# Kernel optimization log

Hardware: AMD Instinct MI355X
Metric: run time of the kernel (lower is better)

The kernel has to match this reference:

```python
import jax, jax.numpy as jnp
import numpy as np

EPS = 1e-5
K = 20


def _knn_idx(p, k):
    # p: (B, N, C) -> indices of k nearest neighbors (B, N, k), self included
    inner = jnp.einsum('bnc,bmc->bnm', p, p)
    sq = jnp.sum(p * p, axis=-1)  # (B, N)
    neg_dist = 2.0 * inner - sq[:, :, None] - sq[:, None, :]
    return jax.lax.top_k(neg_dist, k)[1]


def _edge_feature(x, k):
    # x: (B, N, C) -> (B, N, k, 2C) = [neighbor - center, center]
    C = x.shape[-1]
    src = x if C in (3, 6) else x[..., 6:9]  # faithful to torch code path
    idx = _knn_idx(src, k)                    # (B, N, k)
    nb = jax.vmap(lambda xb, ib: xb[ib])(x, idx)  # (B, N, k, C)
    ctr = jnp.broadcast_to(x[:, :, None, :], nb.shape)
    return jnp.concatenate([nb - ctr, ctr], axis=-1)


def _block(h, W, g, b, m, v):
    # 1x1 conv (channels-last) + eval-mode BatchNorm + LeakyReLU(0.2)
    z = jnp.einsum('...c,oc->...o', h, W)
    z = (z - m) * jax.lax.rsqrt(v + EPS) * g + b
    return jnp.where(z >= 0, z, 0.2 * z)


def setup_inputs() -> dict:
    key = jax.random.key(0)
    B, N, D, F = 8, 2048, 3, 1024
    ks = jax.random.split(key, 16)
    s = 0.1
    x = jax.random.normal(ks[0], (B, N, D), dtype=jnp.float32)
    W1 = jax.random.normal(ks[1], (64, 2 * D), dtype=jnp.float32) * s
    W2 = jax.random.normal(ks[2], (64, 64), dtype=jnp.float32) * s
    W3 = jax.random.normal(ks[3], (64, 128), dtype=jnp.float32) * s
    W4 = jax.random.normal(ks[4], (64, 64), dtype=jnp.float32) * s
    W5 = jax.random.normal(ks[5], (64, 128), dtype=jnp.float32) * s
    W6 = jax.random.normal(ks[6], (F, 192), dtype=jnp.float32) * s
    # BN params for bn1..bn5 stacked along axis 0
    bng = 1.0 + 0.1 * jax.random.normal(ks[7], (5, 64), dtype=jnp.float32)
    bnb = 0.1 * jax.random.normal(ks[8], (5, 64), dtype=jnp.float32)
    bnm = 0.1 * jax.random.normal(ks[9], (5, 64), dtype=jnp.float32)
    bnv = 0.5 + jax.random.uniform(ks[10], (5, 64), dtype=jnp.float32)
    bn6g = 1.0 + 0.1 * jax.random.normal(ks[11], (F,), dtype=jnp.float32)
    bn6b = 0.1 * jax.random.normal(ks[12], (F,), dtype=jnp.float32)
    bn6m = 0.1 * jax.random.normal(ks[13], (F,), dtype=jnp.float32)
    bn6v = 0.5 + jax.random.uniform(ks[14], (F,), dtype=jnp.float32)
    return {"x": x, "W1": W1, "W2": W2, "W3": W3, "W4": W4, "W5": W5,
            "W6": W6, "bng": bng, "bnb": bnb, "bnm": bnm, "bnv": bnv,
            "bn6g": bn6g, "bn6b": bn6b, "bn6m": bn6m, "bn6v": bn6v}


def reference(x, W1, W2, W3, W4, W5, W6, bng, bnb, bnm, bnv,
              bn6g, bn6b, bn6m, bn6v):
    # x: (B, N, 3) channels-last throughout
    e = _edge_feature(x, K)                    # (B, N, K, 6)
    h = _block(e, W1, bng[0], bnb[0], bnm[0], bnv[0])
    h = _block(h, W2, bng[1], bnb[1], bnm[1], bnv[1])
    x1 = jnp.max(h, axis=2)                    # (B, N, 64)

    e = _edge_feature(x1, K)                   # knn on channels 6:9
    h = _block(e, W3, bng[2], bnb[2], bnm[2], bnv[2])
    h = _block(h, W4, bng[3], bnb[3], bnm[3], bnv[3])
    x2 = jnp.max(h, axis=2)                    # (B, N, 64)

    e = _edge_feature(x2, K)
    h = _block(e, W5, bng[4], bnb[4], bnm[4], bnv[4])
    x3 = jnp.max(h, axis=2)                    # (B, N, 64)

    x4 = jnp.concatenate([x1, x2, x3], axis=-1)  # (B, N, 192)
    z = _block(x4, W6, bn6g, bn6b, bn6m, bn6v)   # (B, N, F)
    g = jnp.max(z, axis=1)                       # (B, F)
    feat = g[:, None, :]                         # (B, 1, F)
    return feat, jnp.transpose(x4, (0, 2, 1))    # x4 as (B, 192, N)
```

## Files before the change

### kernel.cpp

```cpp
#include <hip/hip_runtime.h>
#include <hip/hip_bf16.h>
#include <math.h>

#define B_ 8
#define N_ 2048
#define KNN 20
#define CH 64

typedef unsigned int u32;
typedef unsigned short ushort16;
typedef __attribute__((ext_vector_type(8))) short s8v;
typedef __attribute__((ext_vector_type(4))) float f4v;

__device__ __forceinline__ float lrelu(float z) { return z >= 0.0f ? z : 0.2f * z; }

__device__ __forceinline__ u32 enc_f32(float f) {
  u32 u = __float_as_uint(f);
  return (u & 0x80000000u) ? ~u : (u | 0x80000000u);
}
__device__ __forceinline__ float dec_f32(u32 u) {
  u32 bits = (u & 0x80000000u) ? (u ^ 0x80000000u) : ~u;
  return __uint_as_float(bits);
}
__device__ __forceinline__ ushort16 f2bf(float f) {
  u32 u = __float_as_uint(f);
  u = (u + 0x7fffu + ((u >> 16) & 1u)) >> 16;
  return (ushort16)u;
}
__device__ __forceinline__ float bf2f(ushort16 h) { return __uint_as_float(((u32)h) << 16); }

__device__ __forceinline__ void split3(const float* __restrict__ p, s8v& a0, s8v& a1, s8v& a2) {
#pragma unroll
  for (int j = 0; j < 8; ++j) {
    float v = p[j];
    ushort16 h0 = f2bf(v);
    float r = v - bf2f(h0);
    u32 ru = __float_as_uint(r);
    a0[j] = (short)h0;
    a1[j] = (short)(ru >> 16);
    float r2 = r - __uint_as_float(ru & 0xFFFF0000u);
    a2[j] = (short)f2bf(r2);
  }
}

#define MFMA6(ACC, A0, A1, A2, B0, B1, B2)                                   \
  ACC = __builtin_amdgcn_mfma_f32_16x16x32_bf16(A0, B0, ACC, 0, 0, 0);       \
  ACC = __builtin_amdgcn_mfma_f32_16x16x32_bf16(A0, B1, ACC, 0, 0, 0);       \
  ACC = __builtin_amdgcn_mfma_f32_16x16x32_bf16(A1, B0, ACC, 0, 0, 0);       \
  ACC = __builtin_amdgcn_mfma_f32_16x16x32_bf16(A0, B2, ACC, 0, 0, 0);       \
  ACC = __builtin_amdgcn_mfma_f32_16x16x32_bf16(A1, B1, ACC, 0, 0, 0);       \
  ACC = __builtin_amdgcn_mfma_f32_16x16x32_bf16(A2, B0, ACC, 0, 0, 0);

__device__ __forceinline__ void wsplit(float v, ushort16& h0, ushort16& h1, ushort16& h2) {
  h0 = f2bf(v);
  float r = v - bf2f(h0);
  h1 = f2bf(r);
  float r2 = r - bf2f(h1);
  h2 = f2bf(r2);
}

__global__ __launch_bounds__(256) void prep_kernel(
    const float* __restrict__ W2, const float* __restrict__ W3, const float* __restrict__ W4,
    const float* __restrict__ W5, const float* __restrict__ W6,
    float* __restrict__ w2tg, float* __restrict__ w3tg, float* __restrict__ w4tg,
    ushort16* __restrict__ wp5h, ushort16* __restrict__ wp5m, ushort16* __restrict__ wp5l,
    float* __restrict__ w6t, u32* __restrict__ gkeys) {
  int i = blockIdx.x * 256 + threadIdx.x;
  if (i < 192 * 1024) {
    int d = i >> 10, cc = i & 1023;
    w6t[i] = W6[cc * 192 + d];
  }
  if (i < 4096) {
    int c_ = i >> 6, cc = i & 63;
    w2tg[cc * 64 + c_] = W2[i];
    w4tg[cc * 64 + c_] = W4[i];
  }
  if (i < 8192) {
    gkeys[i] = 0u;
    { int d = i >> 6, c_ = i & 63; w3tg[i] = W3[c_ * 128 + d]; }
    int j = i & 7, l = (i >> 3) & 63, tile = i >> 9;
    int kk = tile >> 2, nt = tile & 3;
    int d = kk * 32 + ((l >> 4) << 3) + j;
    int ch = nt * 16 + (l & 15);
    float v5 = (d < 64) ? W5[ch * 128 + d] : (W5[ch * 128 + d] - W5[ch * 128 + d - 64]);
    ushort16 a, b, c;
    wsplit(v5, a, b, c); wp5h[i] = a; wp5m[i] = b; wp5l[i] = c;
  }
}

#define QPB 32
#define SL 8
#define CSL (N_ / SL)
#define CAP 31

__global__ __launch_bounds__(256) void knn_kernel(const float* __restrict__ p, int ld, int off,
                                                  int* __restrict__ idxout) {
  __shared__ __align__(16) char arena[64640];
  float4* pts = (float4*)arena;
  int* buf = (int*)(arena + 32896);
  double* dls = (double*)arena;
  int* ils = (int*)(arena + 40960);

  const int b = blockIdx.y;
  const float* pb = p + (size_t)b * N_ * ld + off;
  for (int j = threadIdx.x; j < N_; j += 256) {
    pts[j + (j >> 8)] = make_float4(pb[(size_t)j * ld + 0], pb[(size_t)j * ld + 1],
                                    pb[(size_t)j * ld + 2], 0.f);
  }
  __syncthreads();

  const int t = threadIdx.x & 7;
  const int qloc = threadIdx.x >> 3;
  const int q = blockIdx.x * QPB + qloc;
  const float4 qp = pts[q + (q >> 8)];
  const int jb = t * CSL;
  const float4* myp = pts + jb + t;

  float d0 = 1e30f, d1 = 1e30f, d2 = 1e30f;
#pragma unroll 4
  for (int i = 0; i < CSL; ++i) {
    float4 c = myp[i];
    float dx = qp.x - c.x, dy = qp.y - c.y, dz = qp.z - c.z;
    float d = fmaf(dz, dz, fmaf(dy, dy, dx * dx));
    float lo = fminf(d, d0); float hi = fmaxf(d, d0); d0 = lo;
    float m1 = fminf(d1, hi); float c1 = fmaxf(d1, hi); d1 = m1;
    d2 = fminf(d2, c1);
  }
  float thr = d2;
#pragma unroll
  for (int s = 1; s < 8; s <<= 1) thr = fmaxf(thr, __shfl_xor(thr, s));
  thr = thr * 1.0001f + 1e-7f;

  int cnt = 0;
  int* mybuf = buf + threadIdx.x * CAP;
#pragma unroll 4
  for (int i = 0; i < CSL; ++i) {
    float4 c = myp[i];
    float dx = qp.x - c.x, dy = qp.y - c.y, dz = qp.z - c.z;
    float d = fmaf(dz, dz, fmaf(dy, dy, dx * dx));
    if (d <= thr) {
      if (cnt < CAP) mybuf[cnt] = jb + i;
      ++cnt;
    }
  }

  double ld_[KNN]; int li_[KNN];
#pragma unroll
  for (int u = 0; u < KNN; ++u) { ld_[u] = 1e300; li_[u] = 0x7fffffff; }

  const bool ovf = cnt > CAP;
  const int m = ovf ? 0 : cnt;
  for (int e = 0; e < m; ++e) {
    int j = mybuf[e];
    float4 c = pts[j + (j >> 8)];
    double dx = (double)qp.x - (double)c.x;
    double dy = (double)qp.y - (double)c.y;
    double dz = (double)qp.z - (double)c.z;
    double d = dx * dx + dy * dy + dz * dz;
    if (d < ld_[KNN - 1]) {
      ld_[KNN - 1] = d; li_[KNN - 1] = j;
#pragma unroll
      for (int u = KNN - 1; u > 0; --u) {
        if (ld_[u] < ld_[u - 1]) {
          double td = ld_[u]; ld_[u] = ld_[u - 1]; ld_[u - 1] = td;
          int ti = li_[u]; li_[u] = li_[u - 1]; li_[u - 1] = ti;
        }
      }
    }
  }
  if (ovf) {
    for (int i = 0; i < CSL; ++i) {
      int j = jb + i;
      float4 c = myp[i];
      double dx = (double)qp.x - (double)c.x;
      double dy = (double)qp.y - (double)c.y;
      double dz = (double)qp.z - (double)c.z;
      double d = dx * dx + dy * dy + dz * dz;
      if (d < ld_[KNN - 1]) {
        ld_[KNN - 1] = d; li_[KNN - 1] = j;
#pragma unroll
        for (int u = KNN - 1; u > 0; --u) {
          if (ld_[u] < ld_[u - 1]) {
            double td = ld_[u]; ld_[u] = ld_[u - 1]; ld_[u - 1] = td;
            int ti = li_[u]; li_[u] = li_[u - 1]; li_[u - 1] = ti;
          }
        }
      }
    }
  }
  __syncthreads();
#pragma unroll
  for (int u = 0; u < KNN; ++u) {
    dls[threadIdx.x * KNN + u] = ld_[u];
    ils[threadIdx.x * KNN + u] = li_[u];
  }
  __syncthreads();

  if (t == 0) {
    int h0 = 0, h1 = 0, h2 = 0, h3 = 0, h4 = 0, h5 = 0, h6 = 0, h7 = 0;
    const int lb = qloc * 8;
    int* outp = idxout + ((size_t)b * N_ + q) * KNN;
    for (int r = 0; r < KNN; ++r) {
      double bd = 1e301; int bi = 0x7fffffff; int bt = 0;
#define CONSIDER(T, H)                                                     \
      { int li2 = (lb + (T)) * KNN + (H);                                  \
        double dv = dls[li2]; int iv = ils[li2];                           \
        if (dv < bd || (dv == bd && iv < bi)) { bd = dv; bi = iv; bt = (T); } }
      CONSIDER(0, h0) CONSIDER(1, h1) CONSIDER(2, h2) CONSIDER(3, h3)
      CONSIDER(4, h4) CONSIDER(5, h5) CONSIDER(6, h6) CONSIDER(7, h7)
#undef CONSIDER
      outp[r] = bi;
      h0 += (bt == 0); h1 += (bt == 1); h2 += (bt == 2); h3 += (bt == 3);
      h4 += (bt == 4); h5 += (bt == 5); h6 += (bt == 6); h7 += (bt == 7);
    }
  }
}

__global__ __launch_bounds__(256) void stage1_kernel(
    const float* __restrict__ x, const int* __restrict__ idx,
    const float* __restrict__ W1, const float* __restrict__ w2tg,
    const float* __restrict__ g0, const float* __restrict__ b0,
    const float* __restrict__ m0, const float* __restrict__ v0,
    const float* __restrict__ g1, const float* __restrict__ b1,
    const float* __restrict__ m1, const float* __restrict__ v1,
    float* __restrict__ x1out) {
  __shared__ float nbs[4][KNN][3];
  __shared__ float ctrs[4][3];
  __shared__ int sidx[4][KNN];
  const int b = blockIdx.y;
  const int n0 = blockIdx.x * 4;
  const int p = threadIdx.x >> 6, c = threadIdx.x & 63;

  for (int i = threadIdx.x; i < 4 * KNN; i += 256)
    sidx[i / KNN][i % KNN] = idx[((size_t)b * N_ + n0 + i / KNN) * KNN + i % KNN];
  __syncthreads();
  for (int i = threadIdx.x; i < 4 * KNN * 3; i += 256) {
    int pp = i / (KNN * 3), r = i % (KNN * 3), k = r / 3, d = r % 3;
    nbs[pp][k][d] = x[((size_t)b * N_ + sidx[pp][k]) * 3 + d];
  }
  if (threadIdx.x < 12) {
    int pp = threadIdx.x / 3, d = threadIdx.x % 3;
    ctrs[pp][d] = x[((size_t)b * N_ + n0 + pp) * 3 + d];
  }
  __syncthreads();

  float sc0, sh0, sc1, sh1;
  {
    double rs = 1.0 / sqrt((double)v0[c] + 1e-5);
    sc0 = (float)((double)g0[c] * rs); sh0 = b0[c] - m0[c] * sc0;
    rs = 1.0 / sqrt((double)v1[c] + 1e-5);
    sc1 = (float)((double)g1[c] * rs); sh1 = b1[c] - m1[c] * sc1;
  }

  const float cx = ctrs[p][0], cy = ctrs[p][1], cz = ctrs[p][2];
  const float wa0 = W1[c * 6 + 0], wa1 = W1[c * 6 + 1], wa2 = W1[c * 6 + 2];
  const float wb0 = W1[c * 6 + 3], wb1 = W1[c * 6 + 4], wb2 = W1[c * 6 + 5];
  const float cbase = cx * wb0 + cy * wb1 + cz * wb2;

  float h1r[KNN];
#pragma unroll
  for (int k = 0; k < KNN; ++k) {
    float a = (nbs[p][k][0] - cx) * wa0 + (nbs[p][k][1] - cy) * wa1 + (nbs[p][k][2] - cz) * wa2 + cbase;
    h1r[k] = lrelu(a * sc0 + sh0);
  }

  float acc2[KNN];
#pragma unroll
  for (int k = 0; k < KNN; ++k) acc2[k] = 0.f;
  for (int cc = 0; cc < CH; ++cc) {
    float w = w2tg[cc * CH + c];
#pragma unroll
    for (int k = 0; k < KNN; ++k) {
      float hv = __int_as_float(__builtin_amdgcn_readlane(__float_as_int(h1r[k]), cc));
      acc2[k] += hv * w;
    }
  }
  float mx = -INFINITY;
#pragma unroll
  for (int k = 0; k < KNN; ++k) mx = fmaxf(mx, lrelu(acc2[k] * sc1 + sh1));
  x1out[((size_t)b * N_ + n0 + p) * CH + c] = mx;
}

__global__ __launch_bounds__(256) void stage2_kernel(
    const float* __restrict__ xin, const int* __restrict__ idx,
    const float* __restrict__ w3tg, const float* __restrict__ w4tg,
    const float* __restrict__ g0, const float* __restrict__ b0,
    const float* __restrict__ m0, const float* __restrict__ v0,
    const float* __restrict__ g1, const float* __restrict__ b1,
    const float* __restrict__ m1, const float* __restrict__ v1,
    float* __restrict__ xout) {
  __shared__ float nbs[4][KNN][CH];
  __shared__ float ctrs[4][CH];
  __shared__ int sidx[4][KNN];
  const int b = blockIdx.y, n0 = blockIdx.x * 4;
  const int p = threadIdx.x >> 6, c = threadIdx.x & 63;

  for (int i = threadIdx.x; i < 4 * KNN; i += 256)
    sidx[i / KNN][i % KNN] = idx[((size_t)b * N_ + n0 + i / KNN) * KNN + i % KNN];
  __syncthreads();
  for (int i = threadIdx.x; i < 4 * KNN * 16; i += 256) {
    int pp = i / (KNN * 16), r = i % (KNN * 16), k = r >> 4, d4 = (r & 15) * 4;
    const float4 v = *(const float4*)&xin[((size_t)b * N_ + sidx[pp][k]) * CH + d4];
    *(float4*)&nbs[pp][k][d4] = v;
  }
  for (int i = threadIdx.x; i < 4 * 16; i += 256) {
    int pp = i / 16, d4 = (i % 16) * 4;
    *(float4*)&ctrs[pp][d4] = *(const float4*)&xin[((size_t)b * N_ + n0 + pp) * CH + d4];
  }
  __syncthreads();

  float sc0, sh0, sc1, sh1;
  {
    double rs = 1.0 / sqrt((double)v0[c] + 1e-5);
    sc0 = (float)((double)g0[c] * rs); sh0 = b0[c] - m0[c] * sc0;
    rs = 1.0 / sqrt((double)v1[c] + 1e-5);
    sc1 = (float)((double)g1[c] * rs); sh1 = b1[c] - m1[c] * sc1;
  }

  float acc[KNN];
#pragma unroll
  for (int k = 0; k < KNN; ++k) acc[k] = 0.f;
  float base = 0.f;
#pragma unroll 4
  for (int d = 0; d < CH; d += 4) {
    float a0 = w3tg[(d + 0) * 64 + c], a1 = w3tg[(d + 1) * 64 + c];
    float a2 = w3tg[(d + 2) * 64 + c], a3 = w3tg[(d + 3) * 64 + c];
    float q0 = w3tg[(64 + d + 0) * 64 + c], q1 = w3tg[(64 + d + 1) * 64 + c];
    float q2 = w3tg[(64 + d + 2) * 64 + c], q3 = w3tg[(64 + d + 3) * 64 + c];
    const float4 ct = *(const float4*)&ctrs[p][d];
    base += ct.x * (q0 - a0) + ct.y * (q1 - a1) + ct.z * (q2 - a2) + ct.w * (q3 - a3);
#pragma unroll
    for (int k = 0; k < KNN; ++k) {
      const float4 nb = *(const float4*)&nbs[p][k][d];
      acc[k] += nb.x * a0 + nb.y * a1 + nb.z * a2 + nb.w * a3;
    }
  }
  float h1r[KNN];
#pragma unroll
  for (int k = 0; k < KNN; ++k) h1r[k] = lrelu((acc[k] + base) * sc0 + sh0);

  float acc2[KNN];
#pragma unroll
  for (int k = 0; k < KNN; ++k) acc2[k] = 0.f;
  for (int cc = 0; cc < CH; ++cc) {
    float w = w4tg[cc * CH + c];
#pragma unroll
    for (int k = 0; k < KNN; ++k) {
      float hv = __int_as_float(__builtin_amdgcn_readlane(__float_as_int(h1r[k]), cc));
      acc2[k] += hv * w;
    }
  }
  float mx = -INFINITY;
#pragma unroll
  for (int k = 0; k < KNN; ++k) mx = fmaxf(mx, lrelu(acc2[k] * sc1 + sh1));
  xout[((size_t)b * N_ + n0 + p) * CH + c] = mx;
}

__global__ __launch_bounds__(256) void stage3_kernel(
    const float* __restrict__ xf, const int* __restrict__ idx,
    const ushort16* __restrict__ wpAh, const ushort16* __restrict__ wpAm, const ushort16* __restrict__ wpAl,
    const float* __restrict__ g0, const float* __restrict__ b0,
    const float* __restrict__ m0, const float* __restrict__ v0,
    float* __restrict__ xoutf) {
  __shared__ int sidx[160];
  __shared__ u32 h2k[512];
  const int b = blockIdx.y, n0 = blockIdx.x * 8;
  const int tid = threadIdx.x, l = tid & 63, wv = tid >> 6;

  for (int i = tid; i < 160; i += 256) sidx[i] = idx[((size_t)b * N_ + n0 + i / KNN) * KNN + i % KNN];
  for (int i = tid; i < 512; i += 256) h2k[i] = 0u;
  __syncthreads();

  float sc1[4], sh1[4];
#pragma unroll
  for (int nt = 0; nt < 4; ++nt) {
    int ch = nt * 16 + (l & 15);
    double rs = 1.0 / sqrt((double)v0[ch] + 1e-5);
    sc1[nt] = (float)((double)g0[ch] * rs); sh1[nt] = b0[ch] - m0[ch] * sc1[nt];
  }
  const int lg = (l >> 4) << 3;

  for (int mt = wv; mt < 10; mt += 4) {
    const int row = mt * 16 + (l & 15);
    const int nb = sidx[row];
    const int p = row / KNN;
    const float* xnb = xf + ((size_t)b * N_ + nb) * CH;
    const float* xct = xf + ((size_t)b * N_ + n0 + p) * CH;

    f4v acc[4];
#pragma unroll
    for (int nt = 0; nt < 4; ++nt) acc[nt] = (f4v){0.f, 0.f, 0.f, 0.f};
#pragma unroll
    for (int kk = 0; kk < 4; ++kk) {
      const float* src = (kk < 2) ? (xnb + kk * 32 + lg) : (xct + (kk - 2) * 32 + lg);
      s8v a0, a1, a2;
      split3(src, a0, a1, a2);
#pragma unroll
      for (int nt = 0; nt < 4; ++nt) {
        int wo = ((kk * 4 + nt) * 64 + l) << 3;
        s8v bh = *(const s8v*)&wpAh[wo];
        s8v bm = *(const s8v*)&wpAm[wo];
        s8v bl = *(const s8v*)&wpAl[wo];
        MFMA6(acc[nt], a0, a1, a2, bh, bm, bl)
      }
    }
#pragma unroll
    for (int nt = 0; nt < 4; ++nt)
#pragma unroll
      for (int r = 0; r < 4; ++r) {
        float v = lrelu(acc[nt][r] * sc1[nt] + sh1[nt]);
        int row2 = mt * 16 + ((l >> 4) << 2) + r;
        atomicMax(&h2k[(row2 / KNN) * 64 + nt * 16 + (l & 15)], enc_f32(v));
      }
  }
  __syncthreads();
  for (int i = tid; i < 512; i += 256) {
    size_t o = ((size_t)b * N_ + n0 + (i >> 6)) * CH + (i & 63);
    xoutf[o] = dec_f32(h2k[i]);
  }
}

__global__ __launch_bounds__(256) void stage6_kernel(
    const float* __restrict__ x1, const float* __restrict__ x2, const float* __restrict__ x3,
    const float* __restrict__ w6t,
    const float* __restrict__ g6, const float* __restrict__ b6,
    const float* __restrict__ m6, const float* __restrict__ v6,
    u32* __restrict__ gkeys) {
  __shared__ float xsT[192][16];
  const int b = blockIdx.y;
  const int n0 = blockIdx.x * 16;
  for (int i = threadIdx.x; i < 16 * 192; i += 256) {
    int d = i >> 4, pp = i & 15;
    float v;
    if (d < 64)       v = x1[((size_t)b * N_ + n0 + pp) * CH + d];
    else if (d < 128) v = x2[((size_t)b * N_ + n0 + pp) * CH + (d - 64)];
    else              v = x3[((size_t)b * N_ + n0 + pp) * CH + (d - 128)];
    xsT[d][pp] = v;
  }
  __syncthreads();

  const int c0 = threadIdx.x << 2;
  float4 acc[16];
#pragma unroll
  for (int pp = 0; pp < 16; ++pp) acc[pp] = make_float4(0.f, 0.f, 0.f, 0.f);

  for (int d = 0; d < 192; ++d) {
    const float4 w = *(const float4*)&w6t[(size_t)d * 1024 + c0];
#pragma unroll
    for (int q = 0; q < 4; ++q) {
      const float4 xq = *(const float4*)&xsT[d][q * 4];
#define ACC4(J, XV) { float4& A = acc[q * 4 + (J)]; A.x += (XV) * w.x; A.y += (XV) * w.y; A.z += (XV) * w.z; A.w += (XV) * w.w; }
      ACC4(0, xq.x) ACC4(1, xq.y) ACC4(2, xq.z) ACC4(3, xq.w)
#undef ACC4
    }
  }

  const float4 gg = *(const float4*)&g6[c0];
  const float4 bb = *(const float4*)&b6[c0];
  const float4 mm = *(const float4*)&m6[c0];
  const float4 vv = *(const float4*)&v6[c0];
  float4 s, h;
  s.x = (float)((double)gg.x / sqrt((double)vv.x + 1e-5)); h.x = bb.x - mm.x * s.x;
  s.y = (float)((double)gg.y / sqrt((double)vv.y + 1e-5)); h.y = bb.y - mm.y * s.y;
  s.z = (float)((double)gg.z / sqrt((double)vv.z + 1e-5)); h.z = bb.z - mm.z * s.z;
  s.w = (float)((double)gg.w / sqrt((double)vv.w + 1e-5)); h.w = bb.w - mm.w * s.w;

  float4 mx = make_float4(-INFINITY, -INFINITY, -INFINITY, -INFINITY);
#pragma unroll
  for (int pp = 0; pp < 16; ++pp) {
    mx.x = fmaxf(mx.x, lrelu(acc[pp].x * s.x + h.x));
    mx.y = fmaxf(mx.y, lrelu(acc[pp].y * s.y + h.y));
    mx.z = fmaxf(mx.z, lrelu(acc[pp].z * s.z + h.z));
    mx.w = fmaxf(mx.w, lrelu(acc[pp].w * s.w + h.w));
  }
  u32* gk = gkeys + (size_t)b * 1024 + c0;
  atomicMax(&gk[0], enc_f32(mx.x));
  atomicMax(&gk[1], enc_f32(mx.y));
  atomicMax(&gk[2], enc_f32(mx.z));
  atomicMax(&gk[3], enc_f32(mx.w));
}

__global__ __launch_bounds__(256) void feat_kernel(const u32* __restrict__ gkeys, float* __restrict__ out) {
  int i = blockIdx.x * 256 + threadIdx.x;
  if (i < 8192) out[i] = dec_f32(gkeys[i]);
}

__global__ __launch_bounds__(256) void xpose_kernel(
    const float* __restrict__ x1, const float* __restrict__ x2, const float* __restrict__ x3,
    float* __restrict__ out) {
  __shared__ float tile[64][65];
  const int b = blockIdx.y;
  const int n0 = blockIdx.x * 64;
  const float* srcs[3] = {x1, x2, x3};
#pragma unroll
  for (int s = 0; s < 3; ++s) {
    const float* src = srcs[s];
    {
      const int row = threadIdx.x >> 2, cb = (threadIdx.x & 3) * 16;
      const float4* rp = (const float4*)&src[((size_t)b * N_ + n0 + row) * CH + cb];
      float4 v0 = rp[0], v1 = rp[1], v2 = rp[2], v3 = rp[3];
      float* tp = &tile[row][cb];
      tp[0] = v0.x; tp[1] = v0.y; tp[2] = v0.z; tp[3] = v0.w;
      tp[4] = v1.x; tp[5] = v1.y; tp[6] = v1.z; tp[7] = v1.w;
      tp[8] = v2.x; tp[9] = v2.y; tp[10] = v2.z; tp[11] = v2.w;
      tp[12] = v3.x; tp[13] = v3.y; tp[14] = v3.z; tp[15] = v3.w;
    }
    __syncthreads();
    {
      const int n = threadIdx.x & 63;
      const int cg = (threadIdx.x >> 6) * 16;
      for (int c = cg; c < cg + 16; ++c)
        out[((size_t)b * 192 + s * 64 + c) * N_ + n0 + n] = tile[n][c];
    }
    __syncthreads();
  }
}

extern "C" void kernel_launch(void* const* d_in, const int* in_sizes, int n_in,
                              void* d_out, int out_size, void* d_ws, size_t ws_size,
                              hipStream_t stream) {
  const float* x   = (const float*)d_in[0];
  const float* W1  = (const float*)d_in[1];
  const float* W2  = (const float*)d_in[2];
  const float* W3  = (const float*)d_in[3];
  const float* W4  = (const float*)d_in[4];
  const float* W5  = (const float*)d_in[5];
  const float* W6  = (const float*)d_in[6];
  const float* bng = (const float*)d_in[7];
  const float* bnb = (const float*)d_in[8];
  const float* bnm = (const float*)d_in[9];
  const float* bnv = (const float*)d_in[10];
  const float* g6  = (const float*)d_in[11];
  const float* b6  = (const float*)d_in[12];
  const float* m6  = (const float*)d_in[13];
  const float* v6  = (const float*)d_in[14];
  float* out = (float*)d_out;

  float* ws = (float*)d_ws;
  float* x1b  = ws;
  float* x2b  = x1b + 1048576;
  float* x3b  = x2b + 1048576;
  float* w6t  = x3b + 1048576;
  float* w2tg = w6t + 196608;
  float* w4tg = w2tg + 4096;
  float* w3tg = w4tg + 4096;
  u32*   gkeys = (u32*)(w3tg + 8192);
  int*   idxb  = (int*)(gkeys + 8192);
  ushort16* wp5h = (ushort16*)(idxb + 327680);
  ushort16* wp5m = wp5h + 65536;
  ushort16* wp5l = wp5m + 65536;

  prep_kernel<<<768, 256, 0, stream>>>(W2, W3, W4, W5, W6,
                                       w2tg, w3tg, w4tg,
                                       wp5h, wp5m, wp5l, w6t, gkeys);

  knn_kernel<<<dim3(N_ / QPB, B_), 256, 0, stream>>>(x, 3, 0, idxb);
  stage1_kernel<<<dim3(N_ / 4, B_), 256, 0, stream>>>(
      x, idxb, W1, w2tg,
      bng + 0, bnb + 0, bnm + 0, bnv + 0,
      bng + 64, bnb + 64, bnm + 64, bnv + 64, x1b);

  knn_kernel<<<dim3(N_ / QPB, B_), 256, 0, stream>>>(x1b, 64, 6, idxb);
  stage2_kernel<<<dim3(N_ / 4, B_), 256, 0, stream>>>(
      x1b, idxb, w3tg, w4tg,
      bng + 128, bnb + 128, bnm + 128, bnv + 128,
      bng + 192, bnb + 192, bnm + 192, bnv + 192, x2b);

  knn_kernel<<<dim3(N_ / QPB, B_), 256, 0, stream>>>(x2b, 64, 6, idxb);
  stage3_kernel<<<dim3(N_ / 8, B_), 256, 0, stream>>>(
      x2b, idxb, wp5h, wp5m, wp5l,
      bng + 256, bnb + 256, bnm + 256, bnv + 256, x3b);

  stage6_kernel<<<dim3(N_ / 16, B_), 256, 0, stream>>>(x1b, x2b, x3b, w6t, g6, b6, m6, v6, gkeys);
  feat_kernel<<<32, 256, 0, stream>>>(gkeys, out);
  xpose_kernel<<<dim3(N_ / 64, B_), 256, 0, stream>>>(x1b, x2b, x3b, out + 8192);
}
```

Before: 798.7 us.

## Move conv6 to 3-way split bf16 MFMA and stage 64x64 matmuls via LDS float4

The final 192->1024 pointwise conv, previously FP32 FMAs, now runs on bf16 MFMA using a three-term bf16 split of both weights and activations to approximate fp32 accuracy. The weights are pre-packed into the MFMA fragment layout in the prep kernel. The second-layer 64x64 matmuls in stage1 and stage2 now write activations to LDS and read them as float4, replacing per-channel readlane broadcasts, with weights pre-packed as float4. The wp5 buffer spacing is also shrunk to its actual size. This trades FMA and readlane throughput for MFMA work and LDS traffic, and changes rounding slightly.

```diff
diff --git a/kernel.cpp b/kernel.cpp
--- a/kernel.cpp
+++ b/kernel.cpp
@@ -62,22 +62,22 @@
 __global__ __launch_bounds__(256) void prep_kernel(
     const float* __restrict__ W2, const float* __restrict__ W3, const float* __restrict__ W4,
     const float* __restrict__ W5, const float* __restrict__ W6,
-    float* __restrict__ w2tg, float* __restrict__ w3tg, float* __restrict__ w4tg,
+    float4* __restrict__ w2p, float4* __restrict__ w3p, float4* __restrict__ w4p,
     ushort16* __restrict__ wp5h, ushort16* __restrict__ wp5m, ushort16* __restrict__ wp5l,
-    float* __restrict__ w6t, u32* __restrict__ gkeys) {
+    ushort16* __restrict__ wp6h, ushort16* __restrict__ wp6m, ushort16* __restrict__ wp6l,
+    u32* __restrict__ gkeys) {
   int i = blockIdx.x * 256 + threadIdx.x;
-  if (i < 192 * 1024) {
-    int d = i >> 10, cc = i & 1023;
-    w6t[i] = W6[cc * 192 + d];
-  }
-  if (i < 4096) {
-    int c_ = i >> 6, cc = i & 63;
-    w2tg[cc * 64 + c_] = W2[i];
-    w4tg[cc * 64 + c_] = W4[i];
+  if (i < 196608) {
+    int j = i & 7, l = (i >> 3) & 63, t = i >> 9;
+    int kk = t >> 6, nt = t & 63;
+    int d = kk * 32 + ((l >> 4) << 3) + j;
+    int ch = nt * 16 + (l & 15);
+    ushort16 a, b, c;
+    wsplit(W6[ch * 192 + d], a, b, c);
+    wp6h[i] = a; wp6m[i] = b; wp6l[i] = c;
   }
   if (i < 8192) {
     gkeys[i] = 0u;
-    { int d = i >> 6, c_ = i & 63; w3tg[i] = W3[c_ * 128 + d]; }
     int j = i & 7, l = (i >> 3) & 63, tile = i >> 9;
     int kk = tile >> 2, nt = tile & 3;
     int d = kk * 32 + ((l >> 4) << 3) + j;
@@ -85,6 +85,15 @@
     float v5 = (d < 64) ? W5[ch * 128 + d] : (W5[ch * 128 + d] - W5[ch * 128 + d - 64]);
     ushort16 a, b, c;
     wsplit(v5, a, b, c); wp5h[i] = a; wp5m[i] = b; wp5l[i] = c;
+  }
+  if (i < 2048) {
+    int g = i >> 6, c_ = i & 63;
+    w3p[i] = *(const float4*)&W3[c_ * 128 + 4 * g];
+  }
+  if (i < 1024) {
+    int g = i >> 6, c_ = i & 63;
+    w2p[i] = *(const float4*)&W2[c_ * 64 + 4 * g];
+    w4p[i] = *(const float4*)&W4[c_ * 64 + 4 * g];
   }
 }
 
@@ -218,7 +227,7 @@
 
 __global__ __launch_bounds__(256) void stage1_kernel(
     const float* __restrict__ x, const int* __restrict__ idx,
-    const float* __restrict__ W1, const float* __restrict__ w2tg,
+    const float* __restrict__ W1, const float4* __restrict__ w2p,
     const float* __restrict__ g0, const float* __restrict__ b0,
     const float* __restrict__ m0, const float* __restrict__ v0,
     const float* __restrict__ g1, const float* __restrict__ b1,
@@ -227,6 +236,7 @@
   __shared__ float nbs[4][KNN][3];
   __shared__ float ctrs[4][3];
   __shared__ int sidx[4][KNN];
+  __shared__ float h1s[4][KNN * CH];
   const int b = blockIdx.y;
   const int n0 = blockIdx.x * 4;
   const int p = threadIdx.x >> 6, c = threadIdx.x & 63;
@@ -264,15 +274,19 @@
     h1r[k] = lrelu(a * sc0 + sh0);
   }
 
+  float* hp = h1s[p];
+#pragma unroll
+  for (int k = 0; k < KNN; ++k) hp[k * CH + c] = h1r[k];
+
   float acc2[KNN];
 #pragma unroll
   for (int k = 0; k < KNN; ++k) acc2[k] = 0.f;
-  for (int cc = 0; cc < CH; ++cc) {
-    float w = w2tg[cc * CH + c];
+  for (int g = 0; g < 16; ++g) {
+    const float4 w = w2p[g * 64 + c];
 #pragma unroll
     for (int k = 0; k < KNN; ++k) {
-      float hv = __int_as_float(__builtin_amdgcn_readlane(__float_as_int(h1r[k]), cc));
-      acc2[k] += hv * w;
+      const float4 hv = *(const float4*)&hp[k * CH + g * 4];
+      acc2[k] += hv.x * w.x; acc2[k] += hv.y * w.y; acc2[k] += hv.z * w.z; acc2[k] += hv.w * w.w;
     }
   }
   float mx = -INFINITY;
@@ -283,7 +297,7 @@
 
 __global__ __launch_bounds__(256) void stage2_kernel(
     const float* __restrict__ xin, const int* __restrict__ idx,
-    const float* __restrict__ w3tg, const float* __restrict__ w4tg,
+    const float4* __restrict__ w3p, const float4* __restrict__ w4p,
     const float* __restrict__ g0, const float* __restrict__ b0,
     const float* __restrict__ m0, const float* __restrict__ v0,
     const float* __restrict__ g1, const float* __restrict__ b1,
@@ -323,10 +337,10 @@
   float base = 0.f;
 #pragma unroll 4
   for (int d = 0; d < CH; d += 4) {
-    float a0 = w3tg[(d + 0) * 64 + c], a1 = w3tg[(d + 1) * 64 + c];
-    float a2 = w3tg[(d + 2) * 64 + c], a3 = w3tg[(d + 3) * 64 + c];
-    float q0 = w3tg[(64 + d + 0) * 64 + c], q1 = w3tg[(64 + d + 1) * 64 + c];
-    float q2 = w3tg[(64 + d + 2) * 64 + c], q3 = w3tg[(64 + d + 3) * 64 + c];
+    const float4 wa = w3p[(d >> 2) * 64 + c];
+    const float4 wq = w3p[(16 + (d >> 2)) * 64 + c];
+    float a0 = wa.x, a1 = wa.y, a2 = wa.z, a3 = wa.w;
+    float q0 = wq.x, q1 = wq.y, q2 = wq.z, q3 = wq.w;
     const float4 ct = *(const float4*)&ctrs[p][d];
     base += ct.x * (q0 - a0) + ct.y * (q1 - a1) + ct.z * (q2 - a2) + ct.w * (q3 - a3);
 #pragma unroll
@@ -339,15 +353,19 @@
 #pragma unroll
   for (int k = 0; k < KNN; ++k) h1r[k] = lrelu((acc[k] + base) * sc0 + sh0);
 
+  float* hp = &nbs[p][0][0];
+#pragma unroll
+  for (int k = 0; k < KNN; ++k) hp[k * CH + c] = h1r[k];
+
   float acc2[KNN];
 #pragma unroll
   for (int k = 0; k < KNN; ++k) acc2[k] = 0.f;
-  for (int cc = 0; cc < CH; ++cc) {
-    float w = w4tg[cc * CH + c];
+  for (int g = 0; g < 16; ++g) {
+    const float4 w = w4p[g * 64 + c];
 #pragma unroll
     for (int k = 0; k < KNN; ++k) {
-      float hv = __int_as_float(__builtin_amdgcn_readlane(__float_as_int(h1r[k]), cc));
-      acc2[k] += hv * w;
+      const float4 hv = *(const float4*)&hp[k * CH + g * 4];
+      acc2[k] += hv.x * w.x; acc2[k] += hv.y * w.y; acc2[k] += hv.z * w.z; acc2[k] += hv.w * w.w;
     }
   }
   float mx = -INFINITY;
@@ -422,62 +440,56 @@
 
 __global__ __launch_bounds__(256) void stage6_kernel(
     const float* __restrict__ x1, const float* __restrict__ x2, const float* __restrict__ x3,
-    const float* __restrict__ w6t,
+    const ushort16* __restrict__ wp6h, const ushort16* __restrict__ wp6m, const ushort16* __restrict__ wp6l,
     const float* __restrict__ g6, const float* __restrict__ b6,
     const float* __restrict__ m6, const float* __restrict__ v6,
     u32* __restrict__ gkeys) {
-  __shared__ float xsT[192][16];
-  const int b = blockIdx.y;
-  const int n0 = blockIdx.x * 16;
-  for (int i = threadIdx.x; i < 16 * 192; i += 256) {
-    int d = i >> 4, pp = i & 15;
-    float v;
-    if (d < 64)       v = x1[((size_t)b * N_ + n0 + pp) * CH + d];
-    else if (d < 128) v = x2[((size_t)b * N_ + n0 + pp) * CH + (d - 64)];
-    else              v = x3[((size_t)b * N_ + n0 + pp) * CH + (d - 128)];
-    xsT[d][pp] = v;
-  }
-  __syncthreads();
-
-  const int c0 = threadIdx.x << 2;
-  float4 acc[16];
-#pragma unroll
-  for (int pp = 0; pp < 16; ++pp) acc[pp] = make_float4(0.f, 0.f, 0.f, 0.f);
-
-  for (int d = 0; d < 192; ++d) {
-    const float4 w = *(const float4*)&w6t[(size_t)d * 1024 + c0];
-#pragma unroll
-    for (int q = 0; q < 4; ++q) {
-      const float4 xq = *(const float4*)&xsT[d][q * 4];
-#define ACC4(J, XV) { float4& A = acc[q * 4 + (J)]; A.x += (XV) * w.x; A.y += (XV) * w.y; A.z += (XV) * w.z; A.w += (XV) * w.w; }
-      ACC4(0, xq.x) ACC4(1, xq.y) ACC4(2, xq.z) ACC4(3, xq.w)
-#undef ACC4
-    }
-  }
-
-  const float4 gg = *(const float4*)&g6[c0];
-  const float4 bb = *(const float4*)&b6[c0];
-  const float4 mm = *(const float4*)&m6[c0];
-  const float4 vv = *(const float4*)&v6[c0];
-  float4 s, h;
-  s.x = (float)((double)gg.x / sqrt((double)vv.x + 1e-5)); h.x = bb.x - mm.x * s.x;
-  s.y = (float)((double)gg.y / sqrt((double)vv.y + 1e-5)); h.y = bb.y - mm.y * s.y;
-  s.z = (float)((double)gg.z / sqrt((double)vv.z + 1e-5)); h.z = bb.z - mm.z * s.z;
-  s.w = (float)((double)gg.w / sqrt((double)vv.w + 1e-5)); h.w = bb.w - mm.w * s.w;
-
-  float4 mx = make_float4(-INFINITY, -INFINITY, -INFINITY, -INFINITY);
-#pragma unroll
-  for (int pp = 0; pp < 16; ++pp) {
-    mx.x = fmaxf(mx.x, lrelu(acc[pp].x * s.x + h.x));
-    mx.y = fmaxf(mx.y, lrelu(acc[pp].y * s.y + h.y));
-    mx.z = fmaxf(mx.z, lrelu(acc[pp].z * s.z + h.z));
-    mx.w = fmaxf(mx.w, lrelu(acc[pp].w * s.w + h.w));
-  }
-  u32* gk = gkeys + (size_t)b * 1024 + c0;
-  atomicMax(&gk[0], enc_f32(mx.x));
-  atomicMax(&gk[1], enc_f32(mx.y));
-  atomicMax(&gk[2], enc_f32(mx.z));
-  atomicMax(&gk[3], enc_f32(mx.w));
+  const int b = blockIdx.y, n0 = blockIdx.x * 32;
+  const int tid = threadIdx.x, l = tid & 63, wv = tid >> 6;
+  const int r16 = l & 15, lg = (l >> 4) << 3;
+
+  f4v acc[2][16];
+#pragma unroll
+  for (int m = 0; m < 2; ++m)
+#pragma unroll
+    for (int nt = 0; nt < 16; ++nt) acc[m][nt] = (f4v){0.f, 0.f, 0.f, 0.f};
+
+  const float* srcs[3] = {x1, x2, x3};
+#pragma unroll
+  for (int kk = 0; kk < 6; ++kk) {
+    const float* src = srcs[kk >> 1];
+    const int col = ((kk & 1) << 5) + lg;
+    s8v a0[2], a1[2], a2[2];
+#pragma unroll
+    for (int m = 0; m < 2; ++m)
+      split3(src + ((size_t)b * N_ + n0 + m * 16 + r16) * CH + col, a0[m], a1[m], a2[m]);
+#pragma unroll
+    for (int nt = 0; nt < 16; ++nt) {
+      int t = kk * 64 + wv * 16 + nt;
+      int wo = (t * 64 + l) << 3;
+      s8v bh = *(const s8v*)&wp6h[wo];
+      s8v bm = *(const s8v*)&wp6m[wo];
+      s8v bl = *(const s8v*)&wp6l[wo];
+      MFMA6(acc[0][nt], a0[0], a1[0], a2[0], bh, bm, bl)
+      MFMA6(acc[1][nt], a0[1], a1[1], a2[1], bh, bm, bl)
+    }
+  }
+
+#pragma unroll
+  for (int nt = 0; nt < 16; ++nt) {
+    const int ch = (wv * 16 + nt) * 16 + r16;
+    double rs = 1.0 / sqrt((double)v6[ch] + 1e-5);
+    const float sc = (float)((double)g6[ch] * rs);
+    const float sh = b6[ch] - m6[ch] * sc;
+    float mx = -INFINITY;
+#pragma unroll
+    for (int m = 0; m < 2; ++m)
+#pragma unroll
+      for (int r = 0; r < 4; ++r) mx = fmaxf(mx, lrelu(acc[m][nt][r] * sc + sh));
+    mx = fmaxf(mx, __shfl_xor(mx, 16));
+    mx = fmaxf(mx, __shfl_xor(mx, 32));
+    if (l < 16) atomicMax(&gkeys[(size_t)b * 1024 + (wv * 16 + nt) * 16 + l], enc_f32(mx));
+  }
 }
 
 __global__ __launch_bounds__(256) void feat_kernel(const u32* __restrict__ gkeys, float* __restrict__ out) {
@@ -540,29 +552,32 @@
   float* x1b  = ws;
   float* x2b  = x1b + 1048576;
   float* x3b  = x2b + 1048576;
-  float* w6t  = x3b + 1048576;
-  float* w2tg = w6t + 196608;
-  float* w4tg = w2tg + 4096;
-  float* w3tg = w4tg + 4096;
-  u32*   gkeys = (u32*)(w3tg + 8192);
+  u32*   gkeys = (u32*)(x3b + 1048576);
   int*   idxb  = (int*)(gkeys + 8192);
   ushort16* wp5h = (ushort16*)(idxb + 327680);
-  ushort16* wp5m = wp5h + 65536;
-  ushort16* wp5l = wp5m + 65536;
+  ushort16* wp5m = wp5h + 8192;
+  ushort16* wp5l = wp5m + 8192;
+  ushort16* wp6h = wp5l + 8192;
+  ushort16* wp6m = wp6h + 196608;
+  ushort16* wp6l = wp6m + 196608;
+  float4* w2p = (float4*)(wp6l + 196608);
+  float4* w3p = w2p + 1024;
+  float4* w4p = w3p + 2048;
 
   prep_kernel<<<768, 256, 0, stream>>>(W2, W3, W4, W5, W6,
-                                       w2tg, w3tg, w4tg,
-                                       wp5h, wp5m, wp5l, w6t, gkeys);
+                                       w2p, w3p, w4p,
+                                       wp5h, wp5m, wp5l,
+                                       wp6h, wp6m, wp6l, gkeys);
 
   knn_kernel<<<dim3(N_ / QPB, B_), 256, 0, stream>>>(x, 3, 0, idxb);
   stage1_kernel<<<dim3(N_ / 4, B_), 256, 0, stream>>>(
-      x, idxb, W1, w2tg,
+      x, idxb, W1, w2p,
       bng + 0, bnb + 0, bnm + 0, bnv + 0,
       bng + 64, bnb + 64, bnm + 64, bnv + 64, x1b);
 
   knn_kernel<<<dim3(N_ / QPB, B_), 256, 0, stream>>>(x1b, 64, 6, idxb);
   stage2_kernel<<<dim3(N_ / 4, B_), 256, 0, stream>>>(
-      x1b, idxb, w3tg, w4tg,
+      x1b, idxb, w3p, w4p,
       bng + 128, bnb + 128, bnm + 128, bnv + 128,
       bng + 192, bnb + 192, bnm + 192, bnv + 192, x2b);
 
@@ -571,7 +586,8 @@
       x2b, idxb, wp5h, wp5m, wp5l,
       bng + 256, bnb + 256, bnm + 256, bnv + 256, x3b);
 
-  stage6_kernel<<<dim3(N_ / 16, B_), 256, 0, stream>>>(x1b, x2b, x3b, w6t, g6, b6, m6, v6, gkeys);
+  stage6_kernel<<<dim3(N_ / 32, B_), 256, 0, stream>>>(
+      x1b, x2b, x3b, wp6h, wp6m, wp6l, g6, b6, m6, v6, gkeys);
   feat_kernel<<<32, 256, 0, stream>>>(gkeys, out);
   xpose_kernel<<<dim3(N_ / 64, B_), 256, 0, stream>>>(x1b, x2b, x3b, out + 8192);
 }
```

Result: faster. 711.8 us (-10.9%).
